# Kernel optimization log

Hardware: AMD Instinct MI355X
Metric: run time of the kernel (lower is better)

The kernel has to match this reference:

```python
import jax, jax.numpy as jnp
import numpy as np

N_ENT = 50000
N_REL = 237
DIM = 200
BATCH = 1024
N_EDGE_RAW = 400000
WALK_LEN = 3


def _build_graph():
    rng = np.random.default_rng(0)
    src = rng.integers(0, N_ENT, N_EDGE_RAW)
    dst = rng.integers(0, N_ENT, N_EDGE_RAW)
    key = np.unique(src.astype(np.int64) * N_ENT + dst.astype(np.int64))
    row = (key // N_ENT).astype(np.int64)
    col = (key % N_ENT).astype(np.int64)
    # symmetric D^{-1/2} A D^{-1/2} normalization (binary coalesced adjacency)
    deg = np.bincount(row, minlength=N_ENT).astype(np.float64)
    dinv = np.where(deg > 0, deg ** -0.5, 0.0)
    adj_val = (dinv[row] * dinv[col]).astype(np.float32)
    # random walk of length 3 from every node (torch_cluster.random_walk semantics)
    rowptr = np.concatenate([[0], np.cumsum(np.bincount(row, minlength=N_ENT))]).astype(np.int64)
    cur = np.arange(N_ENT)
    walk = [cur]
    for _ in range(WALK_LEN):
        d = rowptr[cur + 1] - rowptr[cur]
        off = np.floor(rng.random(N_ENT) * np.maximum(d, 1)).astype(np.int64)
        idx = np.minimum(rowptr[cur] + off, len(row) - 1)
        nxt = np.where(d > 0, col[idx], cur)
        walk.append(nxt)
        cur = nxt
    walk = np.stack(walk, 1)  # (N, WALK_LEN+1)
    # scatter(rw_adj, 1, walk, 1): binary rows, duplicates collapse; then D^{-1} row-normalize
    rw_key = np.unique(np.repeat(np.arange(N_ENT), WALK_LEN + 1).astype(np.int64) * N_ENT + walk.reshape(-1))
    rw_row = (rw_key // N_ENT).astype(np.int64)
    rw_col = (rw_key % N_ENT).astype(np.int64)
    rw_deg = np.bincount(rw_row, minlength=N_ENT).astype(np.float64)
    rw_val = (1.0 / np.maximum(rw_deg[rw_row], 1.0)).astype(np.float32)
    return row, col, adj_val, rw_row, rw_col, rw_val


def setup_inputs() -> dict:
    row, col, adj_val, rw_row, rw_col, rw_val = _build_graph()
    E = row.shape[0]
    key = jax.random.key(0)
    ks = jax.random.split(key, 12)
    g = 0.05
    return dict(
        entity_emb=jax.random.normal(ks[0], (N_ENT, DIM), jnp.float32) * g,
        rel_emb=jax.random.normal(ks[1], (2 * N_REL, DIM * DIM), jnp.float32) * 0.01,
        node_W1=jax.random.normal(ks[2], (2, DIM, DIM), jnp.float32) * g,
        node_b1=jnp.zeros((2, DIM), jnp.float32),
        node_W2=jax.random.normal(ks[3], (2, DIM, 1), jnp.float32) * g,
        node_b2=jnp.zeros((2, 1), jnp.float32),
        edge_W1=jax.random.normal(ks[4], (2, 2 * DIM, DIM), jnp.float32) * g,
        edge_b1=jnp.zeros((2, DIM), jnp.float32),
        edge_W2=jax.random.normal(ks[5], (2, DIM, 1), jnp.float32) * g,
        edge_b2=jnp.zeros((2, 1), jnp.float32),
        adj_row=jnp.asarray(row), adj_col=jnp.asarray(col), adj_val=jnp.asarray(adj_val),
        rw_row=jnp.asarray(rw_row), rw_col=jnp.asarray(rw_col), rw_val=jnp.asarray(rw_val),
        node_eps=jax.random.uniform(ks[6], (2, N_ENT, 1), jnp.float32),
        edge_eps=jax.random.uniform(ks[7], (2, E, 1), jnp.float32),
        sub=jax.random.randint(ks[8], (BATCH,), 0, N_ENT),
        rel=jax.random.randint(ks[9], (BATCH,), 0, 2 * N_REL),
        obj=jax.random.randint(ks[10], (BATCH,), 0, N_ENT),
        neg_tail=jax.random.randint(ks[11], (BATCH, 2), 0, N_ENT),
    )


def _spmm(row, col, val, x, n):
    # sparse COO (row, col, val) @ dense x, output (n, d)
    return jax.ops.segment_sum(val[:, None] * x[col], row, num_segments=n)


def _gate(logits, u):
    # concrete-gate noise: eps ~ U(bias, 1-bias); sigmoid((logit(eps)+logits)/0.5)
    bias = 1e-4
    eps = (2.0 * bias - 1.0) * u + (1.0 - bias)
    return jax.nn.sigmoid((jnp.log(eps) - jnp.log1p(-eps) + logits) / 0.5)


def reference(entity_emb, rel_emb, node_W1, node_b1, node_W2, node_b2,
              edge_W1, edge_b1, edge_W2, edge_b2,
              adj_row, adj_col, adj_val, rw_row, rw_col, rw_val,
              node_eps, edge_eps, sub, rel, obj, neg_tail):
    n, d = entity_emb.shape
    e0 = entity_emb
    node_masks, edge_masks = [], []
    edge_cat = jnp.concatenate([e0[adj_row], e0[adj_col]], axis=-1)  # (E, 2d)
    for i in range(2):
        h = jax.nn.relu(e0 @ node_W1[i] + node_b1[i])
        node_masks.append(_gate(h @ node_W2[i] + node_b2[i], node_eps[i]))  # (n,1)
        he = jax.nn.relu(edge_cat @ edge_W1[i] + edge_b1[i])
        edge_masks.append(_gate(he @ edge_W2[i] + edge_b2[i], edge_eps[i])[:, 0])  # (E,)
    # node-drop branch: mix self vs random-walk mean-pooled, then GCN propagate
    x_nd = e0
    for i in range(2):
        mp = _spmm(rw_row, rw_col, rw_val, x_nd, n)
        x_nd = node_masks[i] * x_nd + (1.0 - node_masks[i]) * mp
        x_nd = _spmm(adj_row, adj_col, adj_val, x_nd, n)
    # edge-drop branch: rw propagation twice; only the LAST edge mask is applied (as in source)
    x_ed = e0
    new_edge = adj_val
    for i in range(2):
        x_ed = _spmm(rw_row, rw_col, rw_val, x_ed, n)
        new_edge = adj_val * edge_masks[i]
    x_ed = _spmm(adj_row, adj_col, new_edge, x_ed, n)
    # RESCAL scoring against all entities
    lhs1 = e0[sub]                                   # (B, d)
    rel1 = rel_emb[rel].reshape(-1, d, d)            # (B, d, d)
    self_hr = jnp.einsum('bd,bde->be', lhs1, rel1)   # (B, d)
    scores = jax.nn.sigmoid(self_hr @ e0.T)          # (B, n)
    return scores, x_nd, x_ed
```

## Files before the change

### kernel.cpp

```cpp
#include <hip/hip_runtime.h>
#include <math.h>

#define DIMV 200
typedef unsigned short ushort;
typedef unsigned int uint;
typedef __attribute__((ext_vector_type(8))) __bf16  bf16x8;
typedef __attribute__((ext_vector_type(4))) float   f32x4;

static __device__ __forceinline__ int lower_bound(const int* __restrict__ a, int n, int key) {
    int lo = 0, hi = n;
    while (lo < hi) {
        int mid = (lo + hi) >> 1;
        if (a[mid] < key) lo = mid + 1; else hi = mid;
    }
    return lo;
}

static __device__ __forceinline__ float gate_fn(float u, float logit) {
    float ee = fmaf(u, -0.9998f, 0.9999f);
    float g  = (logf(ee) - log1pf(-ee) + logit) * 2.0f;
    return 1.0f / (1.0f + expf(-g));
}

static __device__ __forceinline__ ushort f2bf(float f) {
// ... 87 lines not shown
    {
        const int b = bid;
        if (t < DIMV) lhs[t] = e0[(size_t)sub[b] * DIMV + t];
        __syncthreads();
        if (t >= 224) return;
        if (t < DIMV) {
            const float* R = rel_emb + (size_t)rel[b] * (DIMV * DIMV);
            float acc = 0.f;
            for (int dd = 0; dd < DIMV; dd++)
                acc = fmaf(lhs[dd], R[dd * DIMV + t], acc);
            hrbf[(size_t)b * 224 + t] = f2bf(acc);
        } else {
            hrbf[(size_t)b * 224 + t] = 0;
        }
    }
}

__global__ __launch_bounds__(256) void fused_mlp(
    const ushort* __restrict__ e0bf, const ushort* __restrict__ W1eT,
    const ushort* __restrict__ W1nT, ushort* __restrict__ Pb,
    const float* __restrict__ nb1, const float* __restrict__ nW2,
    const float* __restrict__ nb2, const float* __restrict__ neps,
    float* __restrict__ node_mask, int N, int GX)
{
    __shared__ __align__(16) ushort As[2][128 * 40];
    __shared__ __align__(16) ushort Bs[2][208 * 40];
    __shared__ float bsh[208], wsh[208];

    const int r8  = blockIdx.x & 7;
    const int rem = blockIdx.x >> 3;
    const int y   = rem & 3;
    const int q4  = rem >> 2;
    const int x   = r8 + 8 * q4;
    if (x >= GX) return;

    const int t    = threadIdx.x;
    const int lane = t & 63;
    const int w    = t >> 6;
    const int q    = lane >> 4;
    const int ln   = lane & 15;
    const int r0   = x * 128;
    const bool edge = (y < 2);
    const int  i    = y - 2;
    const ushort* Wt = edge ? (W1eT + (size_t)y * 208 * 224)
                            : (W1nT + (size_t)i * 208 * 224);

    if (!edge && t < 208) {
        bsh[t] = (t < 200) ? nb1[i * 200 + t] : 0.f;
        wsh[t] = (t < 200) ? nW2[i * 200 + t] : 0.f;
    }

    f32x4 acc[2][13];
#pragma unroll
    for (int mt = 0; mt < 2; mt++)
#pragma unroll
        for (int nt = 0; nt < 13; nt++) {
            acc[mt][nt][0] = 0.f; acc[mt][nt][1] = 0.f;
            acc[mt][nt][2] = 0.f; acc[mt][nt][3] = 0.f;
        }

    auto stageA = [&](int ks, int buf) {
#pragma unroll
        for (int it = 0; it < 2; it++) {
            int f = t + it * 256;
            int m = f >> 2, c4 = f & 3;
            int g = r0 + m;
            ushort* dst = &As[buf][m * 40 + c4 * 8];
            if (g < N) *(bf16x8*)dst = *(const bf16x8*)&e0bf[(size_t)g * 224 + ks * 32 + c4 * 8];
            else       zero8_store(dst);
        }
    };
    auto stageB = [&](int ks, int buf) {
        for (int f = t; f < 832; f += 256) {
            int n = f >> 2, c4 = f & 3;
            *(bf16x8*)&Bs[buf][n * 40 + c4 * 8] =
                *(const bf16x8*)&Wt[(size_t)n * 224 + ks * 32 + c4 * 8];
        }
    };

    stageA(0, 0); stageB(0, 0);
    __syncthreads();

    for (int ks = 0; ks < 7; ks++) {
        int cur = ks & 1;
        if (ks + 1 < 7) { stageA(ks + 1, cur ^ 1); stageB(ks + 1, cur ^ 1); }
        bf16x8 af0 = *(const bf16x8*)&As[cur][(w * 32 + ln) * 40 + q * 8];
        bf16x8 af1 = *(const bf16x8*)&As[cur][(w * 32 + 16 + ln) * 40 + q * 8];
#pragma unroll
        for (int nt = 0; nt < 13; nt++) {
            bf16x8 bf = *(const bf16x8*)&Bs[cur][(nt * 16 + ln) * 40 + q * 8];
            acc[0][nt] = __builtin_amdgcn_mfma_f32_16x16x32_bf16(af0, bf, acc[0][nt], 0, 0, 0);
            acc[1][nt] = __builtin_amdgcn_mfma_f32_16x16x32_bf16(af1, bf, acc[1][nt], 0, 0, 0);
        }
        __syncthreads();
    }

    if (edge) {
#pragma unroll
        for (int mt = 0; mt < 2; mt++) {
            int gm = r0 + w * 32 + mt * 16 + q * 4;
#pragma unroll
            for (int nt = 0; nt < 13; nt++) {
                int gn = y * 208 + nt * 16 + ln;
                if (gn < 400) {
#pragma unroll
                    for (int r = 0; r < 4; r++)
                        if (gm + r < N) Pb[(size_t)(gm + r) * 400 + gn] = f2bf(acc[mt][nt][r]);
                }
            }
        }
    } else {
        float p[2][4];
#pragma unroll
        for (int mt = 0; mt < 2; mt++)
#pragma unroll
            for (int r = 0; r < 4; r++) {
                float s = 0.f;
#pragma unroll
                for (int nt = 0; nt < 13; nt++) {
                    int n = nt * 16 + ln;
                    float h = fmaxf(acc[mt][nt][r] + bsh[n], 0.f);
                    s = fmaf(h, wsh[n], s);
                }
                p[mt][r] = s;
            }
#pragma unroll
        for (int off = 1; off < 16; off <<= 1)
#pragma unroll
            for (int mt = 0; mt < 2; mt++)
#pragma unroll
                for (int r = 0; r < 4; r++)
                    p[mt][r] += __shfl_xor(p[mt][r], off);

        if (ln == 0) {
            float b2v = nb2[i];
            const float* epsi = neps + (size_t)i * N;
            float* outi = node_mask + (size_t)i * N;
#pragma unroll
            for (int mt = 0; mt < 2; mt++)
#pragma unroll
                for (int r = 0; r < 4; r++) {
                    int g = r0 + w * 32 + mt * 16 + q * 4 + r;
                    if (g < N) outi[g] = gate_fn(epsi[g], p[mt][r] + b2v);
                }
        }
    }
}

static __device__ __forceinline__ void spmm_bb_body(
    const uint* __restrict__ x, int xld, const int* __restrict__ rowptr,
    const int* __restrict__ col, const float* __restrict__ val,
    uint* __restrict__ out, int N, int vb, int t)
{
    const int half = t >> 7;
    const int d2   = t & 127;
    const int r    = vb * 2 + half;
    if (d2 >= 100 || r >= N) return;
    const int lo = rowptr[r], hi = rowptr[r + 1];
    float ax0=0.f,ay0=0.f,ax1=0.f,ay1=0.f,ax2=0.f,ay2=0.f,ax3=0.f,ay3=0.f;
    int e = lo;
    for (; e + 3 < hi; e += 4) {
        int c0=col[e], c1=col[e+1], c2=col[e+2], c3=col[e+3];
        float v0=val[e], v1=val[e+1], v2=val[e+2], v3=val[e+3];
        float2 f0=bfp2f(x[(size_t)c0*xld+d2]);
        float2 f1=bfp2f(x[(size_t)c1*xld+d2]);
        float2 f2=bfp2f(x[(size_t)c2*xld+d2]);
        float2 f3=bfp2f(x[(size_t)c3*xld+d2]);
        ax0=fmaf(v0,f0.x,ax0); ay0=fmaf(v0,f0.y,ay0);
        ax1=fmaf(v1,f1.x,ax1); ay1=fmaf(v1,f1.y,ay1);
        ax2=fmaf(v2,f2.x,ax2); ay2=fmaf(v2,f2.y,ay2);
        ax3=fmaf(v3,f3.x,ax3); ay3=fmaf(v3,f3.y,ay3);
    }
    for (; e < hi; e++) {
        float2 f0=bfp2f(x[(size_t)col[e]*xld+d2]);
        ax0=fmaf(val[e],f0.x,ax0); ay0=fmaf(val[e],f0.y,ay0);
    }
    out[(size_t)r*100+d2] = f2bfp((ax0+ax1)+(ax2+ax3), (ay0+ay1)+(ay2+ay3));
}

static __device__ __forceinline__ void dual_body(
    const uint* __restrict__ xA, const uint* __restrict__ xB,
    const int* __restrict__ rowptr, const int* __restrict__ col,
    const float* __restrict__ val, const float* __restrict__ emask,
    float* __restrict__ outA, uint* __restrict__ outB, int N, int vb, int t)
{
    const int half = t >> 7;
    const int d2   = t & 127;
    const int r    = vb * 2 + half;
    if (d2 >= 100 || r >= N) return;
    const int lo = rowptr[r], hi = rowptr[r + 1];
    float ax0=0.f,ay0=0.f,ax1=0.f,ay1=0.f,ax2=0.f,ay2=0.f,ax3=0.f,ay3=0.f;
    float cx0=0.f,cy0=0.f,cx1=0.f,cy1=0.f,cx2=0.f,cy2=0.f,cx3=0.f,cy3=0.f;
    int e = lo;
    for (; e + 3 < hi; e += 4) {
        size_t o0=(size_t)col[e]*100+d2,   o1=(size_t)col[e+1]*100+d2;
        size_t o2=(size_t)col[e+2]*100+d2, o3=(size_t)col[e+3]*100+d2;
        float v0=val[e], v1=val[e+1], v2=val[e+2], v3=val[e+3];
        float m0=v0*emask[e], m1=v1*emask[e+1], m2=v2*emask[e+2], m3=v3*emask[e+3];
        float2 a0=bfp2f(xA[o0]), a1=bfp2f(xA[o1]), a2=bfp2f(xA[o2]), a3=bfp2f(xA[o3]);
        float2 b0=bfp2f(xB[o0]), b1=bfp2f(xB[o1]), b2=bfp2f(xB[o2]), b3=bfp2f(xB[o3]);
        ax0=fmaf(m0,a0.x,ax0); ay0=fmaf(m0,a0.y,ay0);
        ax1=fmaf(m1,a1.x,ax1); ay1=fmaf(m1,a1.y,ay1);
        ax2=fmaf(m2,a2.x,ax2); ay2=fmaf(m2,a2.y,ay2);
        ax3=fmaf(m3,a3.x,ax3); ay3=fmaf(m3,a3.y,ay3);
        cx0=fmaf(v0,b0.x,cx0); cy0=fmaf(v0,b0.y,cy0);
        cx1=fmaf(v1,b1.x,cx1); cy1=fmaf(v1,b1.y,cy1);
        cx2=fmaf(v2,b2.x,cx2); cy2=fmaf(v2,b2.y,cy2);
        cx3=fmaf(v3,b3.x,cx3); cy3=fmaf(v3,b3.y,cy3);
    }
    for (; e < hi; e++) {
        size_t o0=(size_t)col[e]*100+d2;
        float v0=val[e], m0=v0*emask[e];
        float2 a0=bfp2f(xA[o0]); float2 b0=bfp2f(xB[o0]);
        ax0=fmaf(m0,a0.x,ax0); ay0=fmaf(m0,a0.y,ay0);
        cx0=fmaf(v0,b0.x,cx0); cy0=fmaf(v0,b0.y,cy0);
    }
    float2 oA; oA.x=(ax0+ax1)+(ax2+ax3); oA.y=(ay0+ay1)+(ay2+ay3);
    ((float2*)outA)[(size_t)r*100+d2] = oA;
    outB[(size_t)r*100+d2] = f2bfp((cx0+cx1)+(cx2+cx3), (cy0+cy1)+(cy2+cy3));
}

static __device__ __forceinline__ void rwcomb_body(
    const uint* __restrict__ x, const int* __restrict__ rowptr,
    const int* __restrict__ col, const float* __restrict__ val,
    const float* __restrict__ mask, uint* __restrict__ out, int N, int vb, int t)
{
    const int half = t >> 7;
    const int d2   = t & 127;
    const int r    = vb * 2 + half;
    if (d2 >= 100 || r >= N) return;
    const int lo = rowptr[r], hi = rowptr[r + 1];
    float ax0=0.f,ay0=0.f,ax1=0.f,ay1=0.f,ax2=0.f,ay2=0.f,ax3=0.f,ay3=0.f;
    int e = lo;
    for (; e + 3 < hi; e += 4) {
        int c0=col[e], c1=col[e+1], c2=col[e+2], c3=col[e+3];
        float v0=val[e], v1=val[e+1], v2=val[e+2], v3=val[e+3];
        float2 f0=bfp2f(x[(size_t)c0*100+d2]);
        float2 f1=bfp2f(x[(size_t)c1*100+d2]);
        float2 f2=bfp2f(x[(size_t)c2*100+d2]);
        float2 f3=bfp2f(x[(size_t)c3*100+d2]);
        ax0=fmaf(v0,f0.x,ax0); ay0=fmaf(v0,f0.y,ay0);
        ax1=fmaf(v1,f1.x,ax1); ay1=fmaf(v1,f1.y,ay1);
        ax2=fmaf(v2,f2.x,ax2); ay2=fmaf(v2,f2.y,ay2);
        ax3=fmaf(v3,f3.x,ax3); ay3=fmaf(v3,f3.y,ay3);
    }
    for (; e < hi; e++) {
        float2 f0=bfp2f(x[(size_t)col[e]*100+d2]);
        ax0=fmaf(val[e],f0.x,ax0); ay0=fmaf(val[e],f0.y,ay0);
    }
    const float m = mask[r];
    float2 xs = bfp2f(x[(size_t)r*100+d2]);
    float sx=(ax0+ax1)+(ax2+ax3), sy=(ay0+ay1)+(ay2+ay3);
    out[(size_t)r*100+d2] = f2bfp(fmaf(m, xs.x-sx, sx), fmaf(m, xs.y-sy, sy));
}

static __device__ __forceinline__ void bf32_body(
    const uint* __restrict__ x, const int* __restrict__ rowptr,
    const int* __restrict__ col, const float* __restrict__ val,
    float* __restrict__ out, int N, int vb, int t)
{
    const int half = t >> 7;
    const int d2   = t & 127;
    const int r    = vb * 2 + half;
    if (d2 >= 100 || r >= N) return;
    const int lo = rowptr[r], hi = rowptr[r + 1];
    float ax0=0.f,ay0=0.f,ax1=0.f,ay1=0.f,ax2=0.f,ay2=0.f,ax3=0.f,ay3=0.f;
    int e = lo;
    for (; e + 3 < hi; e += 4) {
        int c0=col[e], c1=col[e+1], c2=col[e+2], c3=col[e+3];
        float v0=val[e], v1=val[e+1], v2=val[e+2], v3=val[e+3];
        float2 f0=bfp2f(x[(size_t)c0*100+d2]);
        float2 f1=bfp2f(x[(size_t)c1*100+d2]);
        float2 f2=bfp2f(x[(size_t)c2*100+d2]);
        float2 f3=bfp2f(x[(size_t)c3*100+d2]);
        ax0=fmaf(v0,f0.x,ax0); ay0=fmaf(v0,f0.y,ay0);
        ax1=fmaf(v1,f1.x,ax1); ay1=fmaf(v1,f1.y,ay1);
        ax2=fmaf(v2,f2.x,ax2); ay2=fmaf(v2,f2.y,ay2);
        ax3=fmaf(v3,f3.x,ax3); ay3=fmaf(v3,f3.y,ay3);
    }
    for (; e < hi; e++) {
        float2 f0=bfp2f(x[(size_t)col[e]*100+d2]);
        ax0=fmaf(val[e],f0.x,ax0); ay0=fmaf(val[e],f0.y,ay0);
    }
    float2 o; o.x=(ax0+ax1)+(ax2+ax3); o.y=(ay0+ay1)+(ay2+ay3);
    ((float2*)out)[(size_t)r*100+d2] = o;
}

static __device__ __forceinline__ void egate_body(
    int vb, int t, const uint* __restrict__ P4, const int* __restrict__ rp_adj,
    const int* __restrict__ adj_col, const float* __restrict__ eps,
    float* __restrict__ edge_mask, int N,
    float bb0x, float bb0y, float bb1x, float bb1y,
    float ww0x, float ww0y, float ww1x, float ww1y, float b2v)
{
    const int lane = t & 63;
    const int w    = t >> 6;
    const int gw   = vb * 4 + w;
    const bool act1 = lane < 36;
    const int r_lo = gw * 2;
    const int r_hi = min(r_lo + 2, N);
    for (int r = r_lo; r < r_hi; r++) {
        const uint* Pr = P4 + (size_t)r * 200;
        float2 a0 = bfp2f(Pr[lane]);
        float2 a1; a1.x = 0.f; a1.y = 0.f;
        if (act1) a1 = bfp2f(Pr[64 + lane]);
        a0.x += bb0x; a0.y += bb0y; a1.x += bb1x; a1.y += bb1y;
        const int lo = rp_adj[r], hi = rp_adj[r + 1];
        int e = lo;
        for (; e + 3 < hi; e += 4) {
            const uint* c0 = P4 + (size_t)adj_col[e]     * 200 + 100;
            const uint* c1 = P4 + (size_t)adj_col[e + 1] * 200 + 100;
            const uint* c2 = P4 + (size_t)adj_col[e + 2] * 200 + 100;
            const uint* c3 = P4 + (size_t)adj_col[e + 3] * 200 + 100;
            float2 q0l=bfp2f(c0[lane]), q1l=bfp2f(c1[lane]),
                   q2l=bfp2f(c2[lane]), q3l=bfp2f(c3[lane]);
            float2 q0h,q1h,q2h,q3h;
            q0h.x=q0h.y=q1h.x=q1h.y=q2h.x=q2h.y=q3h.x=q3h.y=0.f;
            if (act1) {
                q0h=bfp2f(c0[64+lane]); q1h=bfp2f(c1[64+lane]);
                q2h=bfp2f(c2[64+lane]); q3h=bfp2f(c3[64+lane]);
            }
            float s0 = fmaxf(a0.x+q0l.x,0.f)*ww0x + fmaxf(a0.y+q0l.y,0.f)*ww0y
                     + fmaxf(a1.x+q0h.x,0.f)*ww1x + fmaxf(a1.y+q0h.y,0.f)*ww1y;
            float s1 = fmaxf(a0.x+q1l.x,0.f)*ww0x + fmaxf(a0.y+q1l.y,0.f)*ww0y
                     + fmaxf(a1.x+q1h.x,0.f)*ww1x + fmaxf(a1.y+q1h.y,0.f)*ww1y;
            float s2 = fmaxf(a0.x+q2l.x,0.f)*ww0x + fmaxf(a0.y+q2l.y,0.f)*ww0y
                     + fmaxf(a1.x+q2h.x,0.f)*ww1x + fmaxf(a1.y+q2h.y,0.f)*ww1y;
            float s3 = fmaxf(a0.x+q3l.x,0.f)*ww0x + fmaxf(a0.y+q3l.y,0.f)*ww0y
                     + fmaxf(a1.x+q3h.x,0.f)*ww1x + fmaxf(a1.y+q3h.y,0.f)*ww1y;
#pragma unroll
            for (int off = 32; off; off >>= 1) {
                s0 += __shfl_xor(s0, off); s1 += __shfl_xor(s1, off);
                s2 += __shfl_xor(s2, off); s3 += __shfl_xor(s3, off);
            }
            if (lane < 4) {
                float sv = (lane == 0) ? s0 : (lane == 1) ? s1 : (lane == 2) ? s2 : s3;
                edge_mask[e + lane] = gate_fn(eps[e + lane], sv + b2v);
            }
        }
        for (; e < hi; e++) {
            const uint* c0 = P4 + (size_t)adj_col[e] * 200 + 100;
            float2 q0l = bfp2f(c0[lane]);
            float2 q0h; q0h.x = q0h.y = 0.f;
            if (act1) q0h = bfp2f(c0[64 + lane]);
            float s0 = fmaxf(a0.x+q0l.x,0.f)*ww0x + fmaxf(a0.y+q0l.y,0.f)*ww0y
                     + fmaxf(a1.x+q0h.x,0.f)*ww1x + fmaxf(a1.y+q0h.y,0.f)*ww1y;
#pragma unroll
            for (int off = 32; off; off >>= 1) s0 += __shfl_xor(s0, off);
            if (lane == 0) edge_mask[e] = gate_fn(eps[e], s0 + b2v);
        }
    }
}

__global__ __launch_bounds__(256) void k3_rw1_egate(
    const uint* __restrict__ e0u, const int* __restrict__ rp_rw,
    const int* __restrict__ rw_col, const float* __restrict__ rw_val,
    uint* __restrict__ Tb, const uint* __restrict__ P4,
    const int* __restrict__ rp_adj, const int* __restrict__ adj_col,
    const float* __restrict__ eb1, const float* __restrict__ eW2,
    const float* __restrict__ eb2, const float* __restrict__ eeps,
    float* __restrict__ edge_mask, int N, int NB_SP)
{
    int bid = blockIdx.x;
    const int t = threadIdx.x;
    if (bid < NB_SP) { spmm_bb_body(e0u, 112, rp_rw, rw_col, rw_val, Tb, N, bid, t); return; }
    const int lane = t & 63;
    const bool act1 = lane < 36;
    const int dA = 2 * lane, dB = 128 + 2 * lane;
    egate_body(bid - NB_SP, t, P4, rp_adj, adj_col, eeps, edge_mask, N,
               eb1[dA], eb1[dA + 1], act1 ? eb1[dB] : 0.f, act1 ? eb1[dB + 1] : 0.f,
               eW2[dA], eW2[dA + 1], act1 ? eW2[dB] : 0.f, act1 ? eW2[dB + 1] : 0.f,
               eb2[0]);
}

__global__ __launch_bounds__(256) void k4_rw2_combine(
    const uint* __restrict__ Tb, const int* __restrict__ rp_rw,
    const int* __restrict__ rw_col, const float* __restrict__ rw_val,
    uint* __restrict__ T2b, const float* __restrict__ e0,
    const float* __restrict__ mask, uint* __restrict__ xndb, int N, int NB_SP)
{
    int bid = blockIdx.x;
    const int t = threadIdx.x;
    if (bid < NB_SP) { spmm_bb_body(Tb, 100, rp_rw, rw_col, rw_val, T2b, N, bid, t); return; }
    int idx = (bid - NB_SP) * 256 + t;
    if (idx >= N * 100) return;
    float m = mask[idx / 100];
    float2 a = ((const float2*)e0)[idx];
    float2 b = bfp2f(Tb[idx]);
    xndb[idx] = f2bfp(fmaf(m, a.x - b.x, b.x), fmaf(m, a.y - b.y, b.y));
}

__global__ __launch_bounds__(256) void k5_dual(
    const uint* __restrict__ xA, const uint* __restrict__ xB,
    const int* __restrict__ rowptr, const int* __restrict__ col,
    const float* __restrict__ val, const float* __restrict__ emask,
    float* __restrict__ outA, uint* __restrict__ outB, int N)
{
    dual_body(xA, xB, rowptr, col, val, emask, outA, outB, N, blockIdx.x, threadIdx.x);
}

__global__ __launch_bounds__(256) void k6_rwcomb(
    const uint* __restrict__ x, const int* __restrict__ rowptr,
    const int* __restrict__ col, const float* __restrict__ val,
    const float* __restrict__ mask, uint* __restrict__ out, int N)
{
    rwcomb_body(x, rowptr, col, val, mask, out, N, blockIdx.x, threadIdx.x);
}

__global__ __launch_bounds__(256) void k7_bf32(
    const uint* __restrict__ x, const int* __restrict__ rowptr,
    const int* __restrict__ col, const float* __restrict__ val,
    float* __restrict__ out, int N)
{
    bf32_body(x, rowptr, col, val, out, N, blockIdx.x, threadIdx.x);
}

__global__ __launch_bounds__(256) void scores_mfma(
    const ushort* __restrict__ hrbf, const ushort* __restrict__ e0bf,
    float* __restrict__ scores, int Nent, int GX)
{
    __shared__ __align__(16) ushort Bs[2][192 * 40];

    const int r8  = blockIdx.x & 7;
    const int rem = blockIdx.x >> 3;
    const int y   = rem & 7;
    const int q8  = rem >> 3;
    const int x   = r8 + 8 * q8;
    if (x >= GX) return;

    const int t    = threadIdx.x;
    const int lane = t & 63;
    const int w    = t >> 6;
    const int q    = lane >> 4;
    const int ln   = lane & 15;
    const int n0   = x * 192;
    const int b0   = y * 128;
    const int arow = b0 + w * 32 + ln;

    auto stageB = [&](int ks, int buf) {
        for (int f = t; f < 768; f += 256) {
            int n = f >> 2, c4 = f & 3;
            int gn = n0 + n;
            ushort* dst = &Bs[buf][n * 40 + c4 * 8];
            if (gn < Nent) *(bf16x8*)dst = *(const bf16x8*)&e0bf[(size_t)gn * 224 + ks * 32 + c4 * 8];
            else           zero8_store(dst);
        }
    };
    stageB(0, 0);

    f32x4 acc[2][12];
#pragma unroll
    for (int mt = 0; mt < 2; mt++)
#pragma unroll
        for (int nt = 0; nt < 12; nt++) {
            acc[mt][nt][0] = 0.f; acc[mt][nt][1] = 0.f;
            acc[mt][nt][2] = 0.f; acc[mt][nt][3] = 0.f;
        }

    bf16x8 a0 = *(const bf16x8*)&hrbf[(size_t)arow * 224 + q * 8];
    bf16x8 a1 = *(const bf16x8*)&hrbf[(size_t)(arow + 16) * 224 + q * 8];
    __syncthreads();

    for (int ks = 0; ks < 7; ks++) {
        int cur = ks & 1;
        bf16x8 a0n = a0, a1n = a1;
        if (ks + 1 < 7) {
            stageB(ks + 1, cur ^ 1);
            a0n = *(const bf16x8*)&hrbf[(size_t)arow * 224 + (ks + 1) * 32 + q * 8];
            a1n = *(const bf16x8*)&hrbf[(size_t)(arow + 16) * 224 + (ks + 1) * 32 + q * 8];
        }
#pragma unroll
        for (int nt = 0; nt < 12; nt++) {
            bf16x8 bf = *(const bf16x8*)&Bs[cur][(nt * 16 + ln) * 40 + q * 8];
            acc[0][nt] = __builtin_amdgcn_mfma_f32_16x16x32_bf16(a0, bf, acc[0][nt], 0, 0, 0);
            acc[1][nt] = __builtin_amdgcn_mfma_f32_16x16x32_bf16(a1, bf, acc[1][nt], 0, 0, 0);
        }
        __syncthreads();
        a0 = a0n; a1 = a1n;
    }

#pragma unroll
    for (int mt = 0; mt < 2; mt++) {
        int b = b0 + w * 32 + mt * 16 + q * 4;
#pragma unroll
        for (int nt = 0; nt < 12; nt++) {
            int n = n0 + nt * 16 + ln;
            if (n < Nent) {
#pragma unroll
                for (int r = 0; r < 4; r++)
                    scores[(size_t)(b + r) * Nent + n] = 1.f / (1.f + __expf(-acc[mt][nt][r]));
            }
        }
    }
}

extern "C" void kernel_launch(void* const* d_in, const int* in_sizes, int n_in,
                              void* d_out, int out_size, void* d_ws, size_t ws_size,
                              hipStream_t stream)
{
    const float* e0       = (const float*)d_in[0];
    const float* rel_emb  = (const float*)d_in[1];
    const float* node_W1  = (const float*)d_in[2];
    const float* node_b1  = (const float*)d_in[3];
    const float* node_W2  = (const float*)d_in[4];
    const float* node_b2  = (const float*)d_in[5];
    const float* edge_W1  = (const float*)d_in[6];
    const float* edge_b1  = (const float*)d_in[7];
    const float* edge_W2  = (const float*)d_in[8];
    const float* edge_b2  = (const float*)d_in[9];
    const int*   adj_row  = (const int*)d_in[10];
    const int*   adj_col  = (const int*)d_in[11];
    const float* adj_val  = (const float*)d_in[12];
    const int*   rw_row   = (const int*)d_in[13];
    const int*   rw_col   = (const int*)d_in[14];
    const float* rw_val   = (const float*)d_in[15];
    const float* node_eps = (const float*)d_in[16];
    const float* edge_eps = (const float*)d_in[17];
    const int*   sub      = (const int*)d_in[18];
    const int*   rel      = (const int*)d_in[19];

    const int E   = in_sizes[10];
    const int Erw = in_sizes[13];
    const int N   = in_sizes[0] / DIMV;
    const int B   = in_sizes[18];

    ushort* W1eT = (ushort*)d_ws;
    ushort* W1nT = W1eT + 416 * 224;
    ushort* e0bf = W1nT + 2 * 208 * 224;
    ushort* hrbf = e0bf + (size_t)N * 224;
    float*  fb   = (float*)(hrbf + (size_t)B * 224);
    float*  node_mask = fb;
    float*  edge_mask = node_mask + 2 * (size_t)N;
    int*    rp_adj = (int*)(edge_mask + E);
    int*    rp_rw  = rp_adj + (N + 1);

    float* out    = (float*)d_out;
    float* scores = out;
    float* x_nd   = out + (size_t)B * N;
    float* x_ed   = x_nd + (size_t)N * DIMV;
    uint*   Tb   = (uint*)scores;
    uint*   T2b  = Tb   + (size_t)N * 100;
    uint*   xndb = T2b  + (size_t)N * 100;
    uint*   Tnb  = xndb + (size_t)N * 100;
    uint*   Pb   = Tnb  + (size_t)N * 100;

    const int NB_SP = (N + 1) / 2;
    const int EGB   = (N + 7) / 8;
    const int CB    = (N * 100 + 255) / 256;
    const int NB0   = (N * 28 + 255) / 256;
    const int NBr   = (N + 256) / 256;
    const int prep_blocks = NB0 + 364 + 364 + NBr + NBr + B;
    const int GXg = (N + 127) / 128;
    const int GXs = (N + 191) / 192;

    prep_all<<<prep_blocks, 256, 0, stream>>>(
        e0, e0bf, edge_W1 + 400 * 200, W1eT, node_W1, W1nT,
        adj_row, E, rp_adj, rw_row, Erw, rp_rw,
        rel_emb, sub, rel, hrbf, N);

    fused_mlp<<<32 * ((GXg + 7) / 8), 256, 0, stream>>>(
        e0bf, W1eT, W1nT, (ushort*)Pb,
        node_b1, node_W2, node_b2, node_eps, node_mask, N, GXg);

    k3_rw1_egate<<<NB_SP + EGB, 256, 0, stream>>>(
        (const uint*)e0bf, rp_rw, rw_col, rw_val, Tb, Pb, rp_adj, adj_col,
        edge_b1 + 200, edge_W2 + 200, edge_b2 + 1, edge_eps + (size_t)E,
        edge_mask, N, NB_SP);

    k4_rw2_combine<<<NB_SP + CB, 256, 0, stream>>>(
        Tb, rp_rw, rw_col, rw_val, T2b, e0, node_mask, xndb, N, NB_SP);

    k5_dual<<<NB_SP, 256, 0, stream>>>(
        T2b, xndb, rp_adj, adj_col, adj_val, edge_mask, x_ed, Tnb, N);

    k6_rwcomb<<<NB_SP, 256, 0, stream>>>(
        Tnb, rp_rw, rw_col, rw_val, node_mask + N, T2b, N);

    k7_bf32<<<NB_SP, 256, 0, stream>>>(T2b, rp_adj, adj_col, adj_val, x_nd, N);

    scores_mfma<<<64 * ((GXs + 7) / 8), 256, 0, stream>>>(
        hrbf, e0bf, scores, N, GXs);
}
```

Measured before the change: 862.8 us.

## Map one wavefront per row in SpMM kernels with 8-byte vector gathers

All sparse-propagation bodies now assign one 64-lane wavefront per row, with 50 active lanes each loading a uint2 (four bf16 values). Previously two rows shared a 256-thread block using 4-byte loads on 100 lanes. Remainder edges are folded into the main loop with predicated lanes, the bf32 kernel unrolls to 8 edges, and the edge-gate body handles one row per wave with float4 bias and weight loads. The aim is wider memory transactions and fewer idle lanes per gather. The trade-off is more edge-loop iterations per lane and redundant loads for padded edges.

Result: faster. 831.0 us (-3.7%).

```diff
diff --git a/kernel.cpp b/kernel.cpp
--- a/kernel.cpp
+++ b/kernel.cpp
@@ -263,30 +263,37 @@
     const int* __restrict__ col, const float* __restrict__ val,
     uint* __restrict__ out, int N, int vb, int t)
 {
-    const int half = t >> 7;
-    const int d2   = t & 127;
-    const int r    = vb * 2 + half;
-    if (d2 >= 100 || r >= N) return;
+    const int w = t >> 6, lane = t & 63;
+    const int r = vb * 4 + w;
+    if (lane >= 50 || r >= N) return;
+    const int off = 2 * lane;
     const int lo = rowptr[r], hi = rowptr[r + 1];
-    float ax0=0.f,ay0=0.f,ax1=0.f,ay1=0.f,ax2=0.f,ay2=0.f,ax3=0.f,ay3=0.f;
-    int e = lo;
-    for (; e + 3 < hi; e += 4) {
-        int c0=col[e], c1=col[e+1], c2=col[e+2], c3=col[e+3];
-        float v0=val[e], v1=val[e+1], v2=val[e+2], v3=val[e+3];
-        float2 f0=bfp2f(x[(size_t)c0*xld+d2]);
-        float2 f1=bfp2f(x[(size_t)c1*xld+d2]);
-        float2 f2=bfp2f(x[(size_t)c2*xld+d2]);
-        float2 f3=bfp2f(x[(size_t)c3*xld+d2]);
-        ax0=fmaf(v0,f0.x,ax0); ay0=fmaf(v0,f0.y,ay0);
-        ax1=fmaf(v1,f1.x,ax1); ay1=fmaf(v1,f1.y,ay1);
-        ax2=fmaf(v2,f2.x,ax2); ay2=fmaf(v2,f2.y,ay2);
-        ax3=fmaf(v3,f3.x,ax3); ay3=fmaf(v3,f3.y,ay3);
-    }
-    for (; e < hi; e++) {
-        float2 f0=bfp2f(x[(size_t)col[e]*xld+d2]);
-        ax0=fmaf(val[e],f0.x,ax0); ay0=fmaf(val[e],f0.y,ay0);
-    }
-    out[(size_t)r*100+d2] = f2bfp((ax0+ax1)+(ax2+ax3), (ay0+ay1)+(ay2+ay3));
+    float a0 = 0.f, a1 = 0.f, a2 = 0.f, a3 = 0.f;
+    for (int e = lo; e < hi; e += 4) {
+        int n = hi - e;
+        int c0 = col[e];
+        int c1 = n > 1 ? col[e + 1] : c0;
+        int c2 = n > 2 ? col[e + 2] : c0;
+        int c3 = n > 3 ? col[e + 3] : c0;
+        float v0 = val[e];
+        float v1 = n > 1 ? val[e + 1] : 0.f;
+        float v2 = n > 2 ? val[e + 2] : 0.f;
+        float v3 = n > 3 ? val[e + 3] : 0.f;
+        uint2 u0 = *(const uint2*)&x[(size_t)c0 * xld + off];
+        uint2 u1 = *(const uint2*)&x[(size_t)c1 * xld + off];
+        uint2 u2 = *(const uint2*)&x[(size_t)c2 * xld + off];
+        uint2 u3 = *(const uint2*)&x[(size_t)c3 * xld + off];
+        float2 p;
+        p = bfp2f(u0.x); a0 = fmaf(v0, p.x, a0); a1 = fmaf(v0, p.y, a1);
+        p = bfp2f(u0.y); a2 = fmaf(v0, p.x, a2); a3 = fmaf(v0, p.y, a3);
+        p = bfp2f(u1.x); a0 = fmaf(v1, p.x, a0); a1 = fmaf(v1, p.y, a1);
+        p = bfp2f(u1.y); a2 = fmaf(v1, p.x, a2); a3 = fmaf(v1, p.y, a3);
+        p = bfp2f(u2.x); a0 = fmaf(v2, p.x, a0); a1 = fmaf(v2, p.y, a1);
+        p = bfp2f(u2.y); a2 = fmaf(v2, p.x, a2); a3 = fmaf(v2, p.y, a3);
+        p = bfp2f(u3.x); a0 = fmaf(v3, p.x, a0); a1 = fmaf(v3, p.y, a1);
+        p = bfp2f(u3.y); a2 = fmaf(v3, p.x, a2); a3 = fmaf(v3, p.y, a3);
+    }
+    *(uint2*)&out[(size_t)r * 100 + off] = make_uint2(f2bfp(a0, a1), f2bfp(a2, a3));
 }
 
 static __device__ __forceinline__ void dual_body(
@@ -295,40 +302,54 @@
     const float* __restrict__ val, const float* __restrict__ emask,
     float* __restrict__ outA, uint* __restrict__ outB, int N, int vb, int t)
 {
-    const int half = t >> 7;
-    const int d2   = t & 127;
-    const int r    = vb * 2 + half;
-    if (d2 >= 100 || r >= N) return;
+    const int w = t >> 6, lane = t & 63;
+    const int r = vb * 4 + w;
+    if (lane >= 50 || r >= N) return;
+    const int off = 2 * lane;
     const int lo = rowptr[r], hi = rowptr[r + 1];
-    float ax0=0.f,ay0=0.f,ax1=0.f,ay1=0.f,ax2=0.f,ay2=0.f,ax3=0.f,ay3=0.f;
-    float cx0=0.f,cy0=0.f,cx1=0.f,cy1=0.f,cx2=0.f,cy2=0.f,cx3=0.f,cy3=0.f;
-    int e = lo;
-    for (; e + 3 < hi; e += 4) {
-        size_t o0=(size_t)col[e]*100+d2,   o1=(size_t)col[e+1]*100+d2;
-        size_t o2=(size_t)col[e+2]*100+d2, o3=(size_t)col[e+3]*100+d2;
-        float v0=val[e], v1=val[e+1], v2=val[e+2], v3=val[e+3];
-        float m0=v0*emask[e], m1=v1*emask[e+1], m2=v2*emask[e+2], m3=v3*emask[e+3];
-        float2 a0=bfp2f(xA[o0]), a1=bfp2f(xA[o1]), a2=bfp2f(xA[o2]), a3=bfp2f(xA[o3]);
-        float2 b0=bfp2f(xB[o0]), b1=bfp2f(xB[o1]), b2=bfp2f(xB[o2]), b3=bfp2f(xB[o3]);
-        ax0=fmaf(m0,a0.x,ax0); ay0=fmaf(m0,a0.y,ay0);
-        ax1=fmaf(m1,a1.x,ax1); ay1=fmaf(m1,a1.y,ay1);
-        ax2=fmaf(m2,a2.x,ax2); ay2=fmaf(m2,a2.y,ay2);
-        ax3=fmaf(m3,a3.x,ax3); ay3=fmaf(m3,a3.y,ay3);
-        cx0=fmaf(v0,b0.x,cx0); cy0=fmaf(v0,b0.y,cy0);
-        cx1=fmaf(v1,b1.x,cx1); cy1=fmaf(v1,b1.y,cy1);
-        cx2=fmaf(v2,b2.x,cx2); cy2=fmaf(v2,b2.y,cy2);
-        cx3=fmaf(v3,b3.x,cx3); cy3=fmaf(v3,b3.y,cy3);
-    }
-    for (; e < hi; e++) {
-        size_t o0=(size_t)col[e]*100+d2;
-        float v0=val[e], m0=v0*emask[e];
-        float2 a0=bfp2f(xA[o0]); float2 b0=bfp2f(xB[o0]);
-        ax0=fmaf(m0,a0.x,ax0); ay0=fmaf(m0,a0.y,ay0);
-        cx0=fmaf(v0,b0.x,cx0); cy0=fmaf(v0,b0.y,cy0);
-    }
-    float2 oA; oA.x=(ax0+ax1)+(ax2+ax3); oA.y=(ay0+ay1)+(ay2+ay3);
-    ((float2*)outA)[(size_t)r*100+d2] = oA;
-    outB[(size_t)r*100+d2] = f2bfp((cx0+cx1)+(cx2+cx3), (cy0+cy1)+(cy2+cy3));
+    float sA0=0.f,sA1=0.f,sA2=0.f,sA3=0.f;
+    float sB0=0.f,sB1=0.f,sB2=0.f,sB3=0.f;
+    for (int e = lo; e < hi; e += 4) {
+        int n = hi - e;
+        int c0 = col[e];
+        int c1 = n > 1 ? col[e + 1] : c0;
+        int c2 = n > 2 ? col[e + 2] : c0;
+        int c3 = n > 3 ? col[e + 3] : c0;
+        float v0 = val[e];
+        float v1 = n > 1 ? val[e + 1] : 0.f;
+        float v2 = n > 2 ? val[e + 2] : 0.f;
+        float v3 = n > 3 ? val[e + 3] : 0.f;
+        float m0 = v0 * emask[e];
+        float m1 = n > 1 ? v1 * emask[e + 1] : 0.f;
+        float m2 = n > 2 ? v2 * emask[e + 2] : 0.f;
+        float m3 = n > 3 ? v3 * emask[e + 3] : 0.f;
+        size_t o0 = (size_t)c0 * 100 + off, o1 = (size_t)c1 * 100 + off;
+        size_t o2 = (size_t)c2 * 100 + off, o3 = (size_t)c3 * 100 + off;
+        uint2 ua0 = *(const uint2*)&xA[o0], ua1 = *(const uint2*)&xA[o1];
+        uint2 ua2 = *(const uint2*)&xA[o2], ua3 = *(const uint2*)&xA[o3];
+        uint2 ub0 = *(const uint2*)&xB[o0], ub1 = *(const uint2*)&xB[o1];
+        uint2 ub2 = *(const uint2*)&xB[o2], ub3 = *(const uint2*)&xB[o3];
+        float2 p;
+        p = bfp2f(ua0.x); sA0 = fmaf(m0, p.x, sA0); sA1 = fmaf(m0, p.y, sA1);
+        p = bfp2f(ua0.y); sA2 = fmaf(m0, p.x, sA2); sA3 = fmaf(m0, p.y, sA3);
+        p = bfp2f(ua1.x); sA0 = fmaf(m1, p.x, sA0); sA1 = fmaf(m1, p.y, sA1);
+        p = bfp2f(ua1.y); sA2 = fmaf(m1, p.x, sA2); sA3 = fmaf(m1, p.y, sA3);
+        p = bfp2f(ua2.x); sA0 = fmaf(m2, p.x, sA0); sA1 = fmaf(m2, p.y, sA1);
+        p = bfp2f(ua2.y); sA2 = fmaf(m2, p.x, sA2); sA3 = fmaf(m2, p.y, sA3);
+        p = bfp2f(ua3.x); sA0 = fmaf(m3, p.x, sA0); sA1 = fmaf(m3, p.y, sA1);
+        p = bfp2f(ua3.y); sA2 = fmaf(m3, p.x, sA2); sA3 = fmaf(m3, p.y, sA3);
+        p = bfp2f(ub0.x); sB0 = fmaf(v0, p.x, sB0); sB1 = fmaf(v0, p.y, sB1);
+        p = bfp2f(ub0.y); sB2 = fmaf(v0, p.x, sB2); sB3 = fmaf(v0, p.y, sB3);
+        p = bfp2f(ub1.x); sB0 = fmaf(v1, p.x, sB0); sB1 = fmaf(v1, p.y, sB1);
+        p = bfp2f(ub1.y); sB2 = fmaf(v1, p.x, sB2); sB3 = fmaf(v1, p.y, sB3);
+        p = bfp2f(ub2.x); sB0 = fmaf(v2, p.x, sB0); sB1 = fmaf(v2, p.y, sB1);
+        p = bfp2f(ub2.y); sB2 = fmaf(v2, p.x, sB2); sB3 = fmaf(v2, p.y, sB3);
+        p = bfp2f(ub3.x); sB0 = fmaf(v3, p.x, sB0); sB1 = fmaf(v3, p.y, sB1);
+        p = bfp2f(ub3.y); sB2 = fmaf(v3, p.x, sB2); sB3 = fmaf(v3, p.y, sB3);
+    }
+    float4 oA; oA.x = sA0; oA.y = sA1; oA.z = sA2; oA.w = sA3;
+    *(float4*)&outA[(size_t)r * 200 + 2 * off] = oA;
+    *(uint2*)&outB[(size_t)r * 100 + off] = make_uint2(f2bfp(sB0, sB1), f2bfp(sB2, sB3));
 }
 
 static __device__ __forceinline__ void rwcomb_body(
@@ -336,33 +357,42 @@
     const int* __restrict__ col, const float* __restrict__ val,
     const float* __restrict__ mask, uint* __restrict__ out, int N, int vb, int t)
 {
-    const int half = t >> 7;
-    const int d2   = t & 127;
-    const int r    = vb * 2 + half;
-    if (d2 >= 100 || r >= N) return;
+    const int w = t >> 6, lane = t & 63;
+    const int r = vb * 4 + w;
+    if (lane >= 50 || r >= N) return;
+    const int off = 2 * lane;
     const int lo = rowptr[r], hi = rowptr[r + 1];
-    float ax0=0.f,ay0=0.f,ax1=0.f,ay1=0.f,ax2=0.f,ay2=0.f,ax3=0.f,ay3=0.f;
-    int e = lo;
-    for (; e + 3 < hi; e += 4) {
-        int c0=col[e], c1=col[e+1], c2=col[e+2], c3=col[e+3];
-        float v0=val[e], v1=val[e+1], v2=val[e+2], v3=val[e+3];
-        float2 f0=bfp2f(x[(size_t)c0*100+d2]);
-        float2 f1=bfp2f(x[(size_t)c1*100+d2]);
-        float2 f2=bfp2f(x[(size_t)c2*100+d2]);
-        float2 f3=bfp2f(x[(size_t)c3*100+d2]);
-        ax0=fmaf(v0,f0.x,ax0); ay0=fmaf(v0,f0.y,ay0);
-        ax1=fmaf(v1,f1.x,ax1); ay1=fmaf(v1,f1.y,ay1);
-        ax2=fmaf(v2,f2.x,ax2); ay2=fmaf(v2,f2.y,ay2);
-        ax3=fmaf(v3,f3.x,ax3); ay3=fmaf(v3,f3.y,ay3);
-    }
-    for (; e < hi; e++) {
-        float2 f0=bfp2f(x[(size_t)col[e]*100+d2]);
-        ax0=fmaf(val[e],f0.x,ax0); ay0=fmaf(val[e],f0.y,ay0);
+    float a0 = 0.f, a1 = 0.f, a2 = 0.f, a3 = 0.f;
+    for (int e = lo; e < hi; e += 4) {
+        int n = hi - e;
+        int c0 = col[e];
+        int c1 = n > 1 ? col[e + 1] : c0;
+        int c2 = n > 2 ? col[e + 2] : c0;
+        int c3 = n > 3 ? col[e + 3] : c0;
+        float v0 = val[e];
+        float v1 = n > 1 ? val[e + 1] : 0.f;
+        float v2 = n > 2 ? val[e + 2] : 0.f;
+        float v3 = n > 3 ? val[e + 3] : 0.f;
+        uint2 u0 = *(const uint2*)&x[(size_t)c0 * 100 + off];
+        uint2 u1 = *(const uint2*)&x[(size_t)c1 * 100 + off];
+        uint2 u2 = *(const uint2*)&x[(size_t)c2 * 100 + off];
+        uint2 u3 = *(const uint2*)&x[(size_t)c3 * 100 + off];
+        float2 p;
+        p = bfp2f(u0.x); a0 = fmaf(v0, p.x, a0); a1 = fmaf(v0, p.y, a1);
+        p = bfp2f(u0.y); a2 = fmaf(v0, p.x, a2); a3 = fmaf(v0, p.y, a3);
+        p = bfp2f(u1.x); a0 = fmaf(v1, p.x, a0); a1 = fmaf(v1, p.y, a1);
+        p = bfp2f(u1.y); a2 = fmaf(v1, p.x, a2); a3 = fmaf(v1, p.y, a3);
+        p = bfp2f(u2.x); a0 = fmaf(v2, p.x, a0); a1 = fmaf(v2, p.y, a1);
+        p = bfp2f(u2.y); a2 = fmaf(v2, p.x, a2); a3 = fmaf(v2, p.y, a3);
+        p = bfp2f(u3.x); a0 = fmaf(v3, p.x, a0); a1 = fmaf(v3, p.y, a1);
+        p = bfp2f(u3.y); a2 = fmaf(v3, p.x, a2); a3 = fmaf(v3, p.y, a3);
     }
     const float m = mask[r];
-    float2 xs = bfp2f(x[(size_t)r*100+d2]);
-    float sx=(ax0+ax1)+(ax2+ax3), sy=(ay0+ay1)+(ay2+ay3);
-    out[(size_t)r*100+d2] = f2bfp(fmaf(m, xs.x-sx, sx), fmaf(m, xs.y-sy, sy));
+    uint2 xs = *(const uint2*)&x[(size_t)r * 100 + off];
+    float2 xa = bfp2f(xs.x), xb = bfp2f(xs.y);
+    *(uint2*)&out[(size_t)r * 100 + off] = make_uint2(
+        f2bfp(fmaf(m, xa.x - a0, a0), fmaf(m, xa.y - a1, a1)),
+        f2bfp(fmaf(m, xb.x - a2, a2), fmaf(m, xb.y - a3, a3)));
 }
 
 static __device__ __forceinline__ void bf32_body(
@@ -370,95 +400,112 @@
     const int* __restrict__ col, const float* __restrict__ val,
     float* __restrict__ out, int N, int vb, int t)
 {
-    const int half = t >> 7;
-    const int d2   = t & 127;
-    const int r    = vb * 2 + half;
-    if (d2 >= 100 || r >= N) return;
+    const int w = t >> 6, lane = t & 63;
+    const int r = vb * 4 + w;
+    if (lane >= 50 || r >= N) return;
+    const int off = 2 * lane;
     const int lo = rowptr[r], hi = rowptr[r + 1];
-    float ax0=0.f,ay0=0.f,ax1=0.f,ay1=0.f,ax2=0.f,ay2=0.f,ax3=0.f,ay3=0.f;
-    int e = lo;
-    for (; e + 3 < hi; e += 4) {
-        int c0=col[e], c1=col[e+1], c2=col[e+2], c3=col[e+3];
-        float v0=val[e], v1=val[e+1], v2=val[e+2], v3=val[e+3];
-        float2 f0=bfp2f(x[(size_t)c0*100+d2]);
-        float2 f1=bfp2f(x[(size_t)c1*100+d2]);
-        float2 f2=bfp2f(x[(size_t)c2*100+d2]);
-        float2 f3=bfp2f(x[(size_t)c3*100+d2]);
-        ax0=fmaf(v0,f0.x,ax0); ay0=fmaf(v0,f0.y,ay0);
-        ax1=fmaf(v1,f1.x,ax1); ay1=fmaf(v1,f1.y,ay1);
-        ax2=fmaf(v2,f2.x,ax2); ay2=fmaf(v2,f2.y,ay2);
-        ax3=fmaf(v3,f3.x,ax3); ay3=fmaf(v3,f3.y,ay3);
-    }
-    for (; e < hi; e++) {
-        float2 f0=bfp2f(x[(size_t)col[e]*100+d2]);
-        ax0=fmaf(val[e],f0.x,ax0); ay0=fmaf(val[e],f0.y,ay0);
-    }
-    float2 o; o.x=(ax0+ax1)+(ax2+ax3); o.y=(ay0+ay1)+(ay2+ay3);
-    ((float2*)out)[(size_t)r*100+d2] = o;
+    float a0 = 0.f, a1 = 0.f, a2 = 0.f, a3 = 0.f;
+    for (int e = lo; e < hi; e += 8) {
+        int n = hi - e;
+        int c0 = col[e];
+        int c1 = n > 1 ? col[e + 1] : c0;
+        int c2 = n > 2 ? col[e + 2] : c0;
+        int c3 = n > 3 ? col[e + 3] : c0;
+        int c4 = n > 4 ? col[e + 4] : c0;
+        int c5 = n > 5 ? col[e + 5] : c0;
+        int c6 = n > 6 ? col[e + 6] : c0;
+        int c7 = n > 7 ? col[e + 7] : c0;
+        float v0 = val[e];
+        float v1 = n > 1 ? val[e + 1] : 0.f;
+        float v2 = n > 2 ? val[e + 2] : 0.f;
+        float v3 = n > 3 ? val[e + 3] : 0.f;
+        float v4 = n > 4 ? val[e + 4] : 0.f;
+        float v5 = n > 5 ? val[e + 5] : 0.f;
+        float v6 = n > 6 ? val[e + 6] : 0.f;
+        float v7 = n > 7 ? val[e + 7] : 0.f;
+        uint2 u0 = *(const uint2*)&x[(size_t)c0 * 100 + off];
+        uint2 u1 = *(const uint2*)&x[(size_t)c1 * 100 + off];
+        uint2 u2 = *(const uint2*)&x[(size_t)c2 * 100 + off];
+        uint2 u3 = *(const uint2*)&x[(size_t)c3 * 100 + off];
+        uint2 u4 = *(const uint2*)&x[(size_t)c4 * 100 + off];
+        uint2 u5 = *(const uint2*)&x[(size_t)c5 * 100 + off];
+        uint2 u6 = *(const uint2*)&x[(size_t)c6 * 100 + off];
+        uint2 u7 = *(const uint2*)&x[(size_t)c7 * 100 + off];
+        float2 p;
+        p = bfp2f(u0.x); a0 = fmaf(v0, p.x, a0); a1 = fmaf(v0, p.y, a1);
+        p = bfp2f(u0.y); a2 = fmaf(v0, p.x, a2); a3 = fmaf(v0, p.y, a3);
+        p = bfp2f(u1.x); a0 = fmaf(v1, p.x, a0); a1 = fmaf(v1, p.y, a1);
+        p = bfp2f(u1.y); a2 = fmaf(v1, p.x, a2); a3 = fmaf(v1, p.y, a3);
+        p = bfp2f(u2.x); a0 = fmaf(v2, p.x, a0); a1 = fmaf(v2, p.y, a1);
+        p = bfp2f(u2.y); a2 = fmaf(v2, p.x, a2); a3 = fmaf(v2, p.y, a3);
+        p = bfp2f(u3.x); a0 = fmaf(v3, p.x, a0); a1 = fmaf(v3, p.y, a1);
+        p = bfp2f(u3.y); a2 = fmaf(v3, p.x, a2); a3 = fmaf(v3, p.y, a3);
+        p = bfp2f(u4.x); a0 = fmaf(v4, p.x, a0); a1 = fmaf(v4, p.y, a1);
+        p = bfp2f(u4.y); a2 = fmaf(v4, p.x, a2); a3 = fmaf(v4, p.y, a3);
+        p = bfp2f(u5.x); a0 = fmaf(v5, p.x, a0); a1 = fmaf(v5, p.y, a1);
+        p = bfp2f(u5.y); a2 = fmaf(v5, p.x, a2); a3 = fmaf(v5, p.y, a3);
+        p = bfp2f(u6.x); a0 = fmaf(v6, p.x, a0); a1 = fmaf(v6, p.y, a1);
+        p = bfp2f(u6.y); a2 = fmaf(v6, p.x, a2); a3 = fmaf(v6, p.y, a3);
+        p = bfp2f(u7.x); a0 = fmaf(v7, p.x, a0); a1 = fmaf(v7, p.y, a1);
+        p = bfp2f(u7.y); a2 = fmaf(v7, p.x, a2); a3 = fmaf(v7, p.y, a3);
+    }
+    float4 o; o.x = a0; o.y = a1; o.z = a2; o.w = a3;
+    *(float4*)&out[(size_t)r * 200 + 2 * off] = o;
 }
 
 static __device__ __forceinline__ void egate_body(
     int vb, int t, const uint* __restrict__ P4, const int* __restrict__ rp_adj,
     const int* __restrict__ adj_col, const float* __restrict__ eps,
     float* __restrict__ edge_mask, int N,
-    float bb0x, float bb0y, float bb1x, float bb1y,
-    float ww0x, float ww0y, float ww1x, float ww1y, float b2v)
-{
-    const int lane = t & 63;
-    const int w    = t >> 6;
-    const int gw   = vb * 4 + w;
-    const bool act1 = lane < 36;
-    const int r_lo = gw * 2;
-    const int r_hi = min(r_lo + 2, N);
-    for (int r = r_lo; r < r_hi; r++) {
-        const uint* Pr = P4 + (size_t)r * 200;
-        float2 a0 = bfp2f(Pr[lane]);
-        float2 a1; a1.x = 0.f; a1.y = 0.f;
-        if (act1) a1 = bfp2f(Pr[64 + lane]);
-        a0.x += bb0x; a0.y += bb0y; a1.x += bb1x; a1.y += bb1y;
-        const int lo = rp_adj[r], hi = rp_adj[r + 1];
-        int e = lo;
-        for (; e + 3 < hi; e += 4) {
-            const uint* c0 = P4 + (size_t)adj_col[e]     * 200 + 100;
-            const uint* c1 = P4 + (size_t)adj_col[e + 1] * 200 + 100;
-            const uint* c2 = P4 + (size_t)adj_col[e + 2] * 200 + 100;
-            const uint* c3 = P4 + (size_t)adj_col[e + 3] * 200 + 100;
-            float2 q0l=bfp2f(c0[lane]), q1l=bfp2f(c1[lane]),
-                   q2l=bfp2f(c2[lane]), q3l=bfp2f(c3[lane]);
-            float2 q0h,q1h,q2h,q3h;
-            q0h.x=q0h.y=q1h.x=q1h.y=q2h.x=q2h.y=q3h.x=q3h.y=0.f;
-            if (act1) {
-                q0h=bfp2f(c0[64+lane]); q1h=bfp2f(c1[64+lane]);
-                q2h=bfp2f(c2[64+lane]); q3h=bfp2f(c3[64+lane]);
-            }
-            float s0 = fmaxf(a0.x+q0l.x,0.f)*ww0x + fmaxf(a0.y+q0l.y,0.f)*ww0y
-                     + fmaxf(a1.x+q0h.x,0.f)*ww1x + fmaxf(a1.y+q0h.y,0.f)*ww1y;
-            float s1 = fmaxf(a0.x+q1l.x,0.f)*ww0x + fmaxf(a0.y+q1l.y,0.f)*ww0y
-                     + fmaxf(a1.x+q1h.x,0.f)*ww1x + fmaxf(a1.y+q1h.y,0.f)*ww1y;
-            float s2 = fmaxf(a0.x+q2l.x,0.f)*ww0x + fmaxf(a0.y+q2l.y,0.f)*ww0y
-                     + fmaxf(a1.x+q2h.x,0.f)*ww1x + fmaxf(a1.y+q2h.y,0.f)*ww1y;
-            float s3 = fmaxf(a0.x+q3l.x,0.f)*ww0x + fmaxf(a0.y+q3l.y,0.f)*ww0y
-                     + fmaxf(a1.x+q3h.x,0.f)*ww1x + fmaxf(a1.y+q3h.y,0.f)*ww1y;
-#pragma unroll
-            for (int off = 32; off; off >>= 1) {
-                s0 += __shfl_xor(s0, off); s1 += __shfl_xor(s1, off);
-                s2 += __shfl_xor(s2, off); s3 += __shfl_xor(s3, off);
-            }
-            if (lane < 4) {
-                float sv = (lane == 0) ? s0 : (lane == 1) ? s1 : (lane == 2) ? s2 : s3;
-                edge_mask[e + lane] = gate_fn(eps[e + lane], sv + b2v);
-            }
-        }
-        for (; e < hi; e++) {
-            const uint* c0 = P4 + (size_t)adj_col[e] * 200 + 100;
-            float2 q0l = bfp2f(c0[lane]);
-            float2 q0h; q0h.x = q0h.y = 0.f;
-            if (act1) q0h = bfp2f(c0[64 + lane]);
-            float s0 = fmaxf(a0.x+q0l.x,0.f)*ww0x + fmaxf(a0.y+q0l.y,0.f)*ww0y
-                     + fmaxf(a1.x+q0h.x,0.f)*ww1x + fmaxf(a1.y+q0h.y,0.f)*ww1y;
-#pragma unroll
-            for (int off = 32; off; off >>= 1) s0 += __shfl_xor(s0, off);
-            if (lane == 0) edge_mask[e] = gate_fn(eps[e], s0 + b2v);
+    const float* __restrict__ eb1, const float* __restrict__ eW2, float b2v)
+{
+    const int w = t >> 6, lane = t & 63;
+    const int r = vb * 4 + w;
+    if (r >= N) return;
+    const bool act = lane < 50;
+    const int off = act ? 2 * lane : 0;
+    float4 bb, ww;
+    if (act) { bb = *(const float4*)&eb1[4 * lane]; ww = *(const float4*)&eW2[4 * lane]; }
+    else     { bb.x = bb.y = bb.z = bb.w = 0.f; ww.x = ww.y = ww.z = ww.w = 0.f; }
+
+    uint2 pr = *(const uint2*)&P4[(size_t)r * 200 + off];
+    float2 pA = bfp2f(pr.x), pB = bfp2f(pr.y);
+    const float h0 = pA.x + bb.x, h1 = pA.y + bb.y;
+    const float h2 = pB.x + bb.z, h3 = pB.y + bb.w;
+
+    const int lo = rp_adj[r], hi = rp_adj[r + 1];
+    for (int e = lo; e < hi; e += 4) {
+        int n = hi - e;
+        int c0 = adj_col[e];
+        int c1 = n > 1 ? adj_col[e + 1] : c0;
+        int c2 = n > 2 ? adj_col[e + 2] : c0;
+        int c3 = n > 3 ? adj_col[e + 3] : c0;
+        uint2 q0 = *(const uint2*)&P4[(size_t)c0 * 200 + 100 + off];
+        uint2 q1 = *(const uint2*)&P4[(size_t)c1 * 200 + 100 + off];
+        uint2 q2 = *(const uint2*)&P4[(size_t)c2 * 200 + 100 + off];
+        uint2 q3 = *(const uint2*)&P4[(size_t)c3 * 200 + 100 + off];
+        float2 qa, qb;
+        qa = bfp2f(q0.x); qb = bfp2f(q0.y);
+        float s0 = fmaxf(h0 + qa.x, 0.f) * ww.x + fmaxf(h1 + qa.y, 0.f) * ww.y
+                 + fmaxf(h2 + qb.x, 0.f) * ww.z + fmaxf(h3 + qb.y, 0.f) * ww.w;
+        qa = bfp2f(q1.x); qb = bfp2f(q1.y);
+        float s1 = fmaxf(h0 + qa.x, 0.f) * ww.x + fmaxf(h1 + qa.y, 0.f) * ww.y
+                 + fmaxf(h2 + qb.x, 0.f) * ww.z + fmaxf(h3 + qb.y, 0.f) * ww.w;
+        qa = bfp2f(q2.x); qb = bfp2f(q2.y);
+        float s2 = fmaxf(h0 + qa.x, 0.f) * ww.x + fmaxf(h1 + qa.y, 0.f) * ww.y
+                 + fmaxf(h2 + qb.x, 0.f) * ww.z + fmaxf(h3 + qb.y, 0.f) * ww.w;
+        qa = bfp2f(q3.x); qb = bfp2f(q3.y);
+        float s3 = fmaxf(h0 + qa.x, 0.f) * ww.x + fmaxf(h1 + qa.y, 0.f) * ww.y
+                 + fmaxf(h2 + qb.x, 0.f) * ww.z + fmaxf(h3 + qb.y, 0.f) * ww.w;
+#pragma unroll
+        for (int o = 32; o; o >>= 1) {
+            s0 += __shfl_xor(s0, o); s1 += __shfl_xor(s1, o);
+            s2 += __shfl_xor(s2, o); s3 += __shfl_xor(s3, o);
+        }
+        if (lane < 4 && e + lane < hi) {
+            float sv = (lane == 0) ? s0 : (lane == 1) ? s1 : (lane == 2) ? s2 : s3;
+            edge_mask[e + lane] = gate_fn(eps[e + lane], sv + b2v);
         }
     }
 }
@@ -470,30 +517,24 @@
     const int* __restrict__ rp_adj, const int* __restrict__ adj_col,
     const float* __restrict__ eb1, const float* __restrict__ eW2,
     const float* __restrict__ eb2, const float* __restrict__ eeps,
-    float* __restrict__ edge_mask, int N, int NB_SP)
+    float* __restrict__ edge_mask, int N, int NB_CH)
 {
     int bid = blockIdx.x;
     const int t = threadIdx.x;
-    if (bid < NB_SP) { spmm_bb_body(e0u, 112, rp_rw, rw_col, rw_val, Tb, N, bid, t); return; }
-    const int lane = t & 63;
-    const bool act1 = lane < 36;
-    const int dA = 2 * lane, dB = 128 + 2 * lane;
-    egate_body(bid - NB_SP, t, P4, rp_adj, adj_col, eeps, edge_mask, N,
-               eb1[dA], eb1[dA + 1], act1 ? eb1[dB] : 0.f, act1 ? eb1[dB + 1] : 0.f,
-               eW2[dA], eW2[dA + 1], act1 ? eW2[dB] : 0.f, act1 ? eW2[dB + 1] : 0.f,
-               eb2[0]);
+    if (bid < NB_CH) { spmm_bb_body(e0u, 112, rp_rw, rw_col, rw_val, Tb, N, bid, t); return; }
+    egate_body(bid - NB_CH, t, P4, rp_adj, adj_col, eeps, edge_mask, N, eb1, eW2, eb2[0]);
 }
 
 __global__ __launch_bounds__(256) void k4_rw2_combine(
     const uint* __restrict__ Tb, const int* __restrict__ rp_rw,
     const int* __restrict__ rw_col, const float* __restrict__ rw_val,
     uint* __restrict__ T2b, const float* __restrict__ e0,
-    const float* __restrict__ mask, uint* __restrict__ xndb, int N, int NB_SP)
+    const float* __restrict__ mask, uint* __restrict__ xndb, int N, int NB_CH)
 {
     int bid = blockIdx.x;
     const int t = threadIdx.x;
-    if (bid < NB_SP) { spmm_bb_body(Tb, 100, rp_rw, rw_col, rw_val, T2b, N, bid, t); return; }
-    int idx = (bid - NB_SP) * 256 + t;
+    if (bid < NB_CH) { spmm_bb_body(Tb, 100, rp_rw, rw_col, rw_val, T2b, N, bid, t); return; }
+    int idx = (bid - NB_CH) * 256 + t;
     if (idx >= N * 100) return;
     float m = mask[idx / 100];
     float2 a = ((const float2*)e0)[idx];
@@ -655,8 +696,7 @@
     uint*   Tnb  = xndb + (size_t)N * 100;
     uint*   Pb   = Tnb  + (size_t)N * 100;
 
-    const int NB_SP = (N + 1) / 2;
-    const int EGB   = (N + 7) / 8;
+    const int NB_CH = (N + 3) / 4;
     const int CB    = (N * 100 + 255) / 256;
     const int NB0   = (N * 28 + 255) / 256;
     const int NBr   = (N + 256) / 256;
@@ -673,21 +713,21 @@
         e0bf, W1eT, W1nT, (ushort*)Pb,
         node_b1, node_W2, node_b2, node_eps, node_mask, N, GXg);
 
-    k3_rw1_egate<<<NB_SP + EGB, 256, 0, stream>>>(
+    k3_rw1_egate<<<2 * NB_CH, 256, 0, stream>>>(
         (const uint*)e0bf, rp_rw, rw_col, rw_val, Tb, Pb, rp_adj, adj_col,
         edge_b1 + 200, edge_W2 + 200, edge_b2 + 1, edge_eps + (size_t)E,
-        edge_mask, N, NB_SP);
-
-    k4_rw2_combine<<<NB_SP + CB, 256, 0, stream>>>(
-        Tb, rp_rw, rw_col, rw_val, T2b, e0, node_mask, xndb, N, NB_SP);
-
-    k5_dual<<<NB_SP, 256, 0, stream>>>(
+        edge_mask, N, NB_CH);
+
+    k4_rw2_combine<<<NB_CH + CB, 256, 0, stream>>>(
+        Tb, rp_rw, rw_col, rw_val, T2b, e0, node_mask, xndb, N, NB_CH);
+
+    k5_dual<<<NB_CH, 256, 0, stream>>>(
         T2b, xndb, rp_adj, adj_col, adj_val, edge_mask, x_ed, Tnb, N);
 
-    k6_rwcomb<<<NB_SP, 256, 0, stream>>>(
+    k6_rwcomb<<<NB_CH, 256, 0, stream>>>(
         Tnb, rp_rw, rw_col, rw_val, node_mask + N, T2b, N);
 
-    k7_bf32<<<NB_SP, 256, 0, stream>>>(T2b, rp_adj, adj_col, adj_val, x_nd, N);
+    k7_bf32<<<NB_CH, 256, 0, stream>>>(T2b, rp_adj, adj_col, adj_val, x_nd, N);
 
     scores_mfma<<<64 * ((GXs + 7) / 8), 256, 0, stream>>>(
         hrbf, e0bf, scores, N, GXs);
```
